# Optimization experiments

Measured on AMD Instinct MI355X. Metric: run time of the kernel, lower is better.

The kernel has to match this reference:

```python
import jax, jax.numpy as jnp
import numpy as np

# Hyperparameters from init_kwargs
K = 1024           # num_embeddings
D = 256            # embedding_dim
COMMIT = 0.25      # commitment_cost
DECAY = 0.99
LAMBDA = 1e-05
NU = 0.1
TAU = 0.5


def setup_inputs() -> dict:
    key = jax.random.key(0)
    k1, k2, k3 = jax.random.split(key, 3)
    B, H, W = 32, 32, 32
    N = B * H * W
    inputs = jax.random.normal(k1, (B, D, H, W), jnp.float32)
    weight = jax.random.normal(k2, (K, D), jnp.float32) * 0.02  # codebook
    # EMA buffers as initialized on first training step (non-kmeans branch)
    ema_count = jnp.full((K,), N / K, jnp.float32)
    ema_weight = weight * ema_count[:, None]
    # Gumbel noise used by F.gumbel_softmax(-distances, tau, hard=True)
    gumbel_noise = jax.random.gumbel(k3, (N, K), jnp.float32)
    return {"inputs": inputs, "weight": weight, "ema_count": ema_count,
            "ema_weight": ema_weight, "gumbel_noise": gumbel_noise}


def reference(inputs, weight, ema_count, ema_weight, gumbel_noise):
    B, C, H, W = inputs.shape
    # b d h w -> (b h w) d
    x = jnp.transpose(inputs, (0, 2, 3, 1)).reshape(-1, C)  # [N, D]
    N = x.shape[0]

    distances = (jnp.sum(x * x, axis=1, keepdims=True)
                 + jnp.sum(weight * weight, axis=1)
                 - 2.0 * jnp.einsum('nd,kd->nk', x, weight))

    soft_encodings = jax.nn.softmax(-distances / TAU, axis=-1)  # [N, K]

    # Hard gumbel-softmax sample (computed under no_grad in torch):
    # argmax((logits + g)/tau) == argmax(logits + g), logits = -distances
    idx = jnp.argmax(-distances + gumbel_noise, axis=-1)        # [N]
    encodings = jax.nn.one_hot(idx, K, dtype=x.dtype)           # [N, K]

    quantized = (encodings @ weight).reshape(B, H, W, C)        # [B,H,W,D]

    # EMA codebook update (training branch, no_grad)
    new_count = ema_count * DECAY + jnp.sum(soft_encodings, axis=0) * (1.0 - DECAY)
    new_count = (new_count + LAMBDA) / (N + K * LAMBDA) * N
    d_weight = jnp.einsum('nk,nd->kd', soft_encodings, x)
    new_ema_weight = ema_weight * DECAY + d_weight * (1.0 - DECAY)
    new_embedding = new_ema_weight / new_count[:, None]

    # Negative-entropy commitment loss on soft assignments
    probs = soft_encodings
    loss_latents = jnp.mean(jnp.sum(probs * jnp.log(jnp.clip(probs, 1e-08)), axis=-1))
    loss = COMMIT * loss_latents

    # quantized + nu*(quantized - detach(quantized)) == quantized in value
    quantized = quantized + NU * (quantized - jax.lax.stop_gradient(quantized))

    avg_probs = jnp.mean(encodings, axis=0)
    perplexity = jnp.exp(-jnp.sum(avg_probs * jnp.log(avg_probs + 1e-10)))

    quantized_out = jnp.transpose(quantized, (0, 3, 1, 2))  # [B,D,H,W]
    return (loss, quantized_out, perplexity, encodings,
            new_count, new_ema_weight, new_embedding)
```

## Files before the change

kernel.cpp:

```cpp
#include <hip/hip_runtime.h>
#include <math.h>

#define NROWS 32768
#define KCB   1024
#define DDIM  256
#define NHALF 16384

#define O_LOSS 0
#define O_Q    1
#define O_PERP 8388609
#define O_ENC  8388610
#define O_NCNT 41943042
#define O_EMAW 41944066
#define O_EMB  42206210

#define E_XS3   2
#define E_S     12582914

#define W_WSQ  0
#define W_XSQ  1024
#define W_IDX  33792
#define W_COL  66560
#define W_HCNT 67584
#define W_BENT 68608
#define W_NCNT 76800
#define W_T2I  77824
#define W_WB   143360

typedef __attribute__((ext_vector_type(8))) short bf16x8;
typedef __attribute__((ext_vector_type(4))) float f32x4;

#define GLOAD_LDS16(g, l) __builtin_amdgcn_global_load_lds( \
    (const __attribute__((address_space(1))) unsigned int*)(g), \
    (__attribute__((address_space(3))) unsigned int*)(l), 16, 0, 0)

__device__ __forceinline__ float wred_sum(float v) {
#pragma unroll
  for (int off = 32; off > 0; off >>= 1) v += __shfl_xor(v, off);
  return v;
}
__device__ __forceinline__ ushort f2bf(float f) {
  union { float f; unsigned u; } c; c.f = f;
  unsigned u = c.u;
  return (ushort)((u + 0x7fffu + ((u >> 16) & 1u)) >> 16);
}
__device__ __forceinline__ float bf2f(ushort h) {
  union { unsigned u; float f; } c; c.u = ((unsigned)h) << 16;
  return c.f;
}

__global__ void k_init(float* __restrict__ hcnt) {
  int i = blockIdx.x * 256 + threadIdx.x;
  if (i < 1024) hcnt[i] = 0.f;
}

__global__ void k_wsplit(const float* __restrict__ w, float* __restrict__ wsq,
                         ushort* __restrict__ WB) {
  int t = threadIdx.x;
  int lane = t & 63, wv = t >> 6;
  int k = blockIdx.x * 4 + wv;
  int d0 = lane * 4;
  float4 v = *(const float4*)&w[(size_t)k * DDIM + d0];
  float s = v.x * v.x + v.y * v.y + v.z * v.z + v.w * v.w;
  s = wred_sum(s);
  if (lane == 0) wsq[k] = s;
  float vv[4] = {v.x, v.y, v.z, v.w};
  union { ushort u[4]; uint2 q; } hh, mm;
#pragma unroll
  for (int q = 0; q < 4; ++q) {
    ushort h = f2bf(vv[q]);
    float r = vv[q] - bf2f(h);
    hh.u[q] = h;
    mm.u[q] = f2bf(r);
  }
  ushort* row = WB + (size_t)k * 768;
  *(uint2*)&row[d0] = hh.q;
  *(uint2*)&row[256 + d0] = hh.q;
  *(uint2*)&row[512 + d0] = mm.q;
}

__global__ __launch_bounds__(256) void k_xsplit(const float* __restrict__ x,
                                                ushort* __restrict__ XS3,
                                                float* __restrict__ xsq) {
  __shared__ __align__(16) ushort sl[32 * 776];
  __shared__ float sq[32 * 9];
  int t = threadIdx.x;
  int b = blockIdx.x >> 5, mt = blockIdx.x & 31;
  int m0 = mt * 32, mloc = t & 31, dgrp = t >> 5;
  const float* xb = x + (size_t)b * DDIM * 1024 + m0 + mloc;
  float s = 0.f;
#pragma unroll
  for (int jj = 0; jj < 8; ++jj) {
    int d0 = dgrp * 32 + jj * 4;
    float vv[4];
#pragma unroll
    for (int q = 0; q < 4; ++q) vv[q] = xb[(size_t)(d0 + q) * 1024];
    union { ushort u[4]; uint2 q; } hh, mi, lo;
#pragma unroll
    for (int q = 0; q < 4; ++q) {
      float v = vv[q];
      ushort h = f2bf(v);
      float r1 = v - bf2f(h);
      ushort m_ = f2bf(r1);
      float r2 = r1 - bf2f(m_);
      hh.u[q] = h; mi.u[q] = m_; lo.u[q] = f2bf(r2);
      s = fmaf(v, v, s);
    }
    int base = mloc * 776;
    *(uint2*)&sl[base + d0] = hh.q;
    *(uint2*)&sl[base + 256 + d0] = mi.q;
    *(uint2*)&sl[base + 512 + d0] = lo.q;
  }
  sq[mloc * 9 + dgrp] = s;
  __syncthreads();
  if (t < 32) {
    float ss = 0.f;
#pragma unroll
    for (int gq = 0; gq < 8; ++gq) ss += sq[t * 9 + gq];
    xsq[b * 1024 + m0 + t] = ss;
  }
  ushort* dst = XS3 + (size_t)(b * 1024 + m0) * 768;
#pragma unroll
  for (int p = 0; p < 12; ++p) {
    int idx = p * 256 + t;
    int row = idx / 96;
    int co = idx - row * 96;
    *(uint4*)&dst[(size_t)row * 768 + co * 8] = *(uint4*)&sl[row * 776 + co * 8];
  }
}

__global__ __launch_bounds__(256) void k_gemm1t(const ushort* __restrict__ XS3h,
                                                const ushort* __restrict__ WB,
                                                const float* __restrict__ wsq,
                                                const float* __restrict__ xsqh,
                                                float* __restrict__ S) {
  __shared__ __align__(16) ushort Asl[2][8192];
  __shared__ __align__(16) ushort Bsl[2][8192];
  __shared__ float xsl[128];
  __shared__ float wsl[128];
  int t = threadIdx.x;
  int kt = blockIdx.x;
  int n0 = blockIdx.y * 128;
  int k0 = kt * 128;
  int l = t & 63, wid = t >> 6;
  int wr = wid >> 1, wc = wid & 1;
  int hi = l >> 4, c = l & 15;

  if (t < 128) { xsl[t] = xsqh[n0 + t]; wsl[t] = wsq[k0 + t]; }

  f32x4 zero = {0.f, 0.f, 0.f, 0.f};
  f32x4 acc[4][4];
#pragma unroll
  for (int i = 0; i < 4; ++i)
#pragma unroll
    for (int j = 0; j < 4; ++j) acc[i][j] = zero;

  const char* XSb = (const char*)XS3h;
  const char* WBb = (const char*)WB;
  int lr = l >> 3;
  int lsw = ((l & 7) ^ lr) << 4;

#define STAGE(s_, b_)                                                              \
  {                                                                                \
    size_t bofs_ = (size_t)(s_) << 7;                                              \
    size_t aofs_ = (size_t)(((s_) < 8) ? (s_) : (s_) - 8) << 7;                    \
    char* Ad_ = (char*)Asl + (b_) * 16384;                                         \
    char* Bd_ = (char*)Bsl + (b_) * 16384;                                         \
    _Pragma("unroll")                                                              \
    for (int q_ = 0; q_ < 4; ++q_) {                                               \
      int seg_ = wid * 32 + q_ * 8;                                                \
      GLOAD_LDS16(XSb + (size_t)(n0 + seg_ + lr) * 1536 + aofs_ + lsw,             \
                  Ad_ + seg_ * 128);                                               \
      GLOAD_LDS16(WBb + (size_t)(k0 + seg_ + lr) * 1536 + bofs_ + lsw,             \
                  Bd_ + seg_ * 128);                                               \
    }                                                                              \
  }

  STAGE(0, 0);
  asm volatile("s_waitcnt vmcnt(0)" ::: "memory");
  __builtin_amdgcn_s_barrier();
  __builtin_amdgcn_sched_barrier(0);

  int buf = 0;
  for (int s = 0; s < 12; ++s) {
    if (s < 11) STAGE(s + 1, buf ^ 1);
    const ushort* Ab = &Asl[buf][0];
    const ushort* Bb = &Bsl[buf][0];
#pragma unroll
    for (int kk = 0; kk < 2; ++kk) {
      bf16x8 af[4], bg[4];
#pragma unroll
      for (int i = 0; i < 4; ++i) {
        int row = wr * 64 + i * 16 + c;
        int ch = (kk * 4 + hi) ^ (row & 7);
        af[i] = *(const bf16x8*)&Ab[row * 64 + ch * 8];
      }
#pragma unroll
      for (int j = 0; j < 4; ++j) {
        int row = wc * 64 + j * 16 + c;
        int ch = (kk * 4 + hi) ^ (row & 7);
        bg[j] = *(const bf16x8*)&Bb[row * 64 + ch * 8];
      }
#pragma unroll
      for (int i = 0; i < 4; ++i)
#pragma unroll
        for (int j = 0; j < 4; ++j)
          acc[i][j] = __builtin_amdgcn_mfma_f32_16x16x32_bf16(af[i], bg[j], acc[i][j], 0, 0, 0);
    }
    asm volatile("s_waitcnt vmcnt(0)" ::: "memory");
    __builtin_amdgcn_s_barrier();
    buf ^= 1;
  }
#undef STAGE

#pragma unroll
  for (int i = 0; i < 4; ++i) {
#pragma unroll
    for (int r = 0; r < 4; ++r) {
      int nl = wr * 64 + i * 16 + hi * 4 + r;
      float xs = xsl[nl];
#pragma unroll
      for (int j = 0; j < 4; ++j) {
        int kl = wc * 64 + j * 16 + c;
        float nd = fmaf(2.f, acc[i][j][r], -(xs + wsl[kl]));
        S[(size_t)(n0 + nl) * 1024 + k0 + kl] = nd;
      }
    }
  }
}

__global__ __launch_bounds__(256) void k_rowops2(float* __restrict__ S,
                                                 const float* __restrict__ Gh,
                                                 float* __restrict__ benth,
                                                 int* __restrict__ t2igh) {
  __shared__ float went[4];
  int t = threadIdx.x;
  int l = t & 63, wv = t >> 6;
  int n = blockIdx.x * 4 + wv;
  float* row = S + ((size_t)n << 10);
  const float* grow = Gh + ((size_t)n << 10);
  float v[16];
  float mx = -3.0e38f;
  float v1 = -3.0e38f, v2 = -3.0e38f;
  int i1 = 0x7fffffff, i2 = 0x7fffffff;
#pragma unroll
  for (int j = 0; j < 4; ++j) {
    float4 a = *(const float4*)&row[j * 256 + l * 4];
    float4 gg = *(const float4*)&grow[j * 256 + l * 4];
    float av[4] = {a.x, a.y, a.z, a.w};
    float gv[4] = {gg.x, gg.y, gg.z, gg.w};
#pragma unroll
    for (int q = 0; q < 4; ++q) {
      v[j * 4 + q] = av[q];
      mx = fmaxf(mx, av[q]);
      float sc = av[q] + gv[q];
      int kk = j * 256 + l * 4 + q;
      if (sc > v1 || (sc == v1 && kk < i1)) { v2 = v1; i2 = i1; v1 = sc; i1 = kk; }
      else if (sc > v2 || (sc == v2 && kk < i2)) { v2 = sc; i2 = kk; }
    }
  }
#pragma unroll
  for (int off = 1; off < 64; off <<= 1) {
    mx = fmaxf(mx, __shfl_xor(mx, off));
    float ov1 = __shfl_xor(v1, off), ov2 = __shfl_xor(v2, off);
    int oi1 = __shfl_xor(i1, off), oi2 = __shfl_xor(i2, off);
    bool fB = (ov1 > v1) || (ov1 == v1 && oi1 < i1);
    float nv1 = fB ? ov1 : v1; int ni1 = fB ? oi1 : i1;
    float ca = fB ? v1 : ov1;  int cia = fB ? i1 : oi1;
    float cb = fB ? ov2 : v2;  int cib = fB ? oi2 : i2;
    bool sB = (cb > ca) || (cb == ca && cib < cia);
    v1 = nv1; i1 = ni1;
    v2 = sB ? cb : ca; i2 = sB ? cib : cia;
  }
  if (l == 0) { t2igh[n * 2] = i1; t2igh[n * 2 + 1] = i2; }

  float M = 2.f * mx;
  float e[16]; float ps = 0.f;
#pragma unroll
  for (int u = 0; u < 16; ++u) { e[u] = __expf(fmaf(2.f, v[u], -M)); ps += e[u]; }
  ps = wred_sum(ps);
  float inv = 1.f / ps;
  float ent = 0.f;
#pragma unroll
  for (int j = 0; j < 4; ++j) {
    float4 o;
    float s0 = e[j * 4 + 0] * inv, s1 = e[j * 4 + 1] * inv;
    float s2 = e[j * 4 + 2] * inv, s3 = e[j * 4 + 3] * inv;
    ent += s0 * __logf(fmaxf(s0, 1e-8f)) + s1 * __logf(fmaxf(s1, 1e-8f));
    ent += s2 * __logf(fmaxf(s2, 1e-8f)) + s3 * __logf(fmaxf(s3, 1e-8f));
    o.x = s0; o.y = s1; o.z = s2; o.w = s3;
    *(float4*)&row[j * 256 + l * 4] = o;
  }
  ent = wred_sum(ent);
  if (l == 0) went[wv] = ent;
  __syncthreads();
  if (t == 0) benth[blockIdx.x] = went[0] + went[1] + went[2] + went[3];
}

__global__ void k_transpose2(const float* __restrict__ soft, ushort* __restrict__ sTp) {
  __shared__ ushort lds[64 * 65];
  int t = threadIdx.x;
  int ktile = blockIdx.x & 15, nt = blockIdx.x >> 4;
  int n0 = nt * 64, k0 = ktile * 64;
#pragma unroll
  for (int p = 0; p < 2; ++p) {
    int row = p * 32 + (t >> 3);
    int c8 = (t & 7) * 8;
    float4 a = *(const float4*)&soft[(size_t)(n0 + row) * 1024 + k0 + c8];
    float4 b = *(const float4*)&soft[(size_t)(n0 + row) * 1024 + k0 + c8 + 4];
    ushort* d = &lds[row * 65 + c8];
    d[0] = f2bf(a.x); d[1] = f2bf(a.y); d[2] = f2bf(a.z); d[3] = f2bf(a.w);
    d[4] = f2bf(b.x); d[5] = f2bf(b.y); d[6] = f2bf(b.z); d[7] = f2bf(b.w);
  }
  __syncthreads();
#pragma unroll
  for (int p = 0; p < 2; ++p) {
    int krow = p * 32 + (t >> 3);
    int nc8 = (t & 7) * 8;
    uint* dst = (uint*)&sTp[(size_t)(k0 + krow) * NHALF + n0 + nc8];
#pragma unroll
    for (int j = 0; j < 4; ++j) {
      uint lo = lds[(nc8 + 2 * j) * 65 + krow];
      uint hh = lds[(nc8 + 2 * j + 1) * 65 + krow];
      dst[j] = lo | (hh << 16);
    }
  }
}

__global__ __launch_bounds__(256) void k_refine(const ushort* __restrict__ XS3,
                                                const float* __restrict__ w,
                                                const float* __restrict__ wsq,
                                                const float* __restrict__ xsq,
                                                const float* __restrict__ G,
                                                const int* __restrict__ t2ig,
                                                int* __restrict__ idxArr,
                                                float* __restrict__ hcnt) {
  int t = threadIdx.x;
  int l = t & 63, wv = t >> 6;
  int base = blockIdx.x * 64 + wv * 16;
  int d0 = l * 4;
  for (int rr = 0; rr < 16; ++rr) {
    int n = base + rr;
    const ushort* p = XS3 + (size_t)n * 768;
    union { uint2 q; ushort u[4]; } ha, ma, la;
    ha.q = *(const uint2*)&p[d0];
    ma.q = *(const uint2*)&p[256 + d0];
    la.q = *(const uint2*)&p[512 + d0];
    float xv[4];
#pragma unroll
    for (int q = 0; q < 4; ++q) xv[q] = bf2f(ha.u[q]) + bf2f(ma.u[q]) + bf2f(la.u[q]);
    float xs = xsq[n];
    int ia = t2ig[n * 2], ib = t2ig[n * 2 + 1];
    float sc[2];
    int ids[2] = {ia, ib};
#pragma unroll
    for (int cdd = 0; cdd < 2; ++cdd) {
      int id = ids[cdd];
      const float* wr = w + (size_t)id * DDIM;
      float4 wv4 = *(const float4*)&wr[d0];
      float d = xv[0] * wv4.x + xv[1] * wv4.y + xv[2] * wv4.z + xv[3] * wv4.w;
      d = wred_sum(d);
      sc[cdd] = fmaf(2.f, d, -xs) - wsq[id] + G[((size_t)n << 10) + id];
    }
    int win = (sc[1] > sc[0] || (sc[1] == sc[0] && ib < ia)) ? ib : ia;
    if (l == 0) {
      idxArr[n] = win;
      atomicAdd(&hcnt[win], 1.f);
    }
  }
}

__global__ void k_quant(const float* __restrict__ w, const int* __restrict__ idxArr,
                        float* __restrict__ outQ) {
  int n = blockIdx.x * 256 + threadIdx.x;
  int b = n >> 10, m = n & 1023;
  int id = idxArr[n];
  const float* wr = w + (size_t)id * DDIM;
  float* o = outQ + (size_t)b * DDIM * 1024 + m;
#pragma unroll 4
  for (int d = 0; d < DDIM; ++d) o[(size_t)d * 1024] = wr[d];
}

__global__ __launch_bounds__(512) void k_gemm2_mfma(const ushort* __restrict__ sT0,
                                                    const ushort* __restrict__ sT1,
                                                    const float* __restrict__ x,
                                                    float* __restrict__ P) {
  __shared__ __align__(16) ushort Abuf[256 * 72];
  __shared__ __align__(16) ushort Bbuf[128 * 72];
  int t = threadIdx.x;
  int bid = blockIdx.x;
  int kt = bid & 3, dt = (bid >> 2) & 1, ns = bid >> 3;
  int k0 = kt * 256, d0 = dt * 128;
  int l = t & 63, wv = t >> 6;
  int wk = wv >> 1, wd = wv & 1;
  const ushort* Abase = (ns < 16) ? sT0 : sT1;
  size_t nloc0 = (size_t)(ns & 15) * 1024;
  f32x4 zero = {0.f, 0.f, 0.f, 0.f};
  f32x4 acc[4][4];
#pragma unroll
  for (int i = 0; i < 4; ++i)
#pragma unroll
    for (int j = 0; j < 4; ++j) acc[i][j] = zero;

  int colv = (t & 7) * 8;
  int rbase = t >> 3;
  for (int s = 0; s < 16; ++s) {
#pragma unroll
    for (int p = 0; p < 4; ++p) {
      int row = p * 64 + rbase;
      const uint* ap = (const uint*)(Abase + (size_t)(k0 + row) * NHALF + nloc0 + s * 64 + colv);
      uint4 v; v.x = ap[0]; v.y = ap[1]; v.z = ap[2]; v.w = ap[3];
      *(uint4*)&Abuf[row * 72 + colv] = v;
    }
#pragma unroll
    for (int p = 0; p < 2; ++p) {
      int row = p * 64 + rbase;
      const float* xp = &x[((size_t)ns * DDIM + d0 + row) * 1024 + s * 64 + colv];
      float4 a = *(const float4*)xp;
      float4 b = *(const float4*)(xp + 4);
      union { ushort u[8]; uint4 q; } pk;
      pk.u[0] = f2bf(a.x); pk.u[1] = f2bf(a.y); pk.u[2] = f2bf(a.z); pk.u[3] = f2bf(a.w);
      pk.u[4] = f2bf(b.x); pk.u[5] = f2bf(b.y); pk.u[6] = f2bf(b.z); pk.u[7] = f2bf(b.w);
      *(uint4*)&Bbuf[row * 72 + colv] = pk.q;
    }
    __syncthreads();
    bf16x8 af[4], bfr[4];
#pragma unroll
    for (int nb2 = 0; nb2 < 2; ++nb2) {
#pragma unroll
      for (int sub = 0; sub < 4; ++sub) {
        af[sub] = *(const bf16x8*)&Abuf[(wk * 64 + sub * 16 + (l & 15)) * 72 + nb2 * 32 + (l >> 4) * 8];
        bfr[sub] = *(const bf16x8*)&Bbuf[(wd * 64 + sub * 16 + (l & 15)) * 72 + nb2 * 32 + (l >> 4) * 8];
      }
#pragma unroll
      for (int i = 0; i < 4; ++i)
#pragma unroll
        for (int j = 0; j < 4; ++j)
          acc[i][j] = __builtin_amdgcn_mfma_f32_16x16x32_bf16(af[i], bfr[j], acc[i][j], 0, 0, 0);
    }
    __syncthreads();
  }
  float* Pb = P + (size_t)ns * (KCB * DDIM);
#pragma unroll
  for (int i = 0; i < 4; ++i)
#pragma unroll
    for (int j = 0; j < 4; ++j) {
#pragma unroll
      for (int r = 0; r < 4; ++r) {
        int k = k0 + wk * 64 + i * 16 + (l >> 4) * 4 + r;
        int d = d0 + wd * 64 + j * 16 + (l & 15);
        Pb[(size_t)k * DDIM + d] = acc[i][j][r];
      }
    }
}

__global__ void k_colsum2(const ushort* __restrict__ sT0, const ushort* __restrict__ sT1,
                          float* __restrict__ colsum) {
  int k = blockIdx.x;
  int t = threadIdx.x;
  const uint* r0 = (const uint*)(sT0 + (size_t)k * NHALF);
  const uint* r1 = (const uint*)(sT1 + (size_t)k * NHALF);
  float s = 0.f;
#pragma unroll
  for (int cc = 0; cc < 8; ++cc) {
#pragma unroll
    for (int q = 0; q < 4; ++q) {
      uint a = r0[cc * 1024 + t * 4 + q];
      uint b = r1[cc * 1024 + t * 4 + q];
      s += bf2f((ushort)(a & 0xffffu)) + bf2f((ushort)(a >> 16));
      s += bf2f((ushort)(b & 0xffffu)) + bf2f((ushort)(b >> 16));
    }
  }
  s = wred_sum(s);
  __shared__ float ws4[4];
  if ((t & 63) == 0) ws4[t >> 6] = s;
  __syncthreads();
  if (t == 0) colsum[k] = ws4[0] + ws4[1] + ws4[2] + ws4[3];
}

__global__ void k_final1(const float* __restrict__ ema_count, const float* __restrict__ colsum,
                         const float* __restrict__ hcnt, const float* __restrict__ bent,
                         float* __restrict__ ncnt, float* __restrict__ out) {
  __shared__ float red[1024];
  int t = threadIdx.x;
  const float onem = 1.0f - 0.99f;
  float nc = ema_count[t] * 0.99f + colsum[t] * onem;
  nc = (nc + 1e-5f) / (32768.0f + 1024.0f * 1e-5f) * 32768.0f;
  out[O_NCNT + t] = nc;
  ncnt[t] = nc;
  float s = 0.f;
  for (int i = t; i < 8192; i += 1024) s += bent[i];
  red[t] = s;
  __syncthreads();
  for (int off = 512; off > 0; off >>= 1) { if (t < off) red[t] += red[t + off]; __syncthreads(); }
  if (t == 0) out[O_LOSS] = 0.25f * (red[0] / 32768.0f);
  __syncthreads();
  float avg = hcnt[t] * (1.0f / 32768.0f);
  red[t] = avg * logf(avg + 1e-10f);
  __syncthreads();
  for (int off = 512; off > 0; off >>= 1) { if (t < off) red[t] += red[t + off]; __syncthreads(); }
  if (t == 0) out[O_PERP] = expf(-red[0]);
}

__global__ void k_reduce_final2(const float* __restrict__ P, const float* __restrict__ ema_w,
                                const float* __restrict__ ncnt, float* __restrict__ outEW,
                                float* __restrict__ outEMB) {
  int i = blockIdx.x * 256 + threadIdx.x;
  float s = 0.f;
#pragma unroll
  for (int ns = 0; ns < 32; ++ns) s += P[(size_t)ns * (KCB * DDIM) + i];
  float ew = ema_w[i] * 0.99f + s * 0.01f;
  outEW[i] = ew;
  outEMB[i] = ew / ncnt[i >> 8];
}

__global__ void k_onehot(const int* __restrict__ idxArr, float* __restrict__ E) {
  int gid = blockIdx.x * 256 + threadIdx.x;
  int n = gid >> 8;
  int k4 = (gid & 255) * 4;
  int id = idxArr[n];
  float2* E2 = (float2*)E;
  size_t base = ((size_t)n * KCB + k4) >> 1;
  float2 vA = {(float)(k4 == id), (float)(k4 + 1 == id)};
  float2 vB = {(float)(k4 + 2 == id), (float)(k4 + 3 == id)};
  E2[base] = vA;
  E2[base + 1] = vB;
}

extern "C" void kernel_launch(void* const* d_in, const int* in_sizes, int n_in,
                              void* d_out, int out_size, void* d_ws, size_t ws_size,
                              hipStream_t stream) {
  const float* x = (const float*)d_in[0];
  const float* w = (const float*)d_in[1];
  const float* ema_count = (const float*)d_in[2];
  const float* ema_w = (const float*)d_in[3];
  const float* g = (const float*)d_in[4];
  float* out = (float*)d_out;
  float* ws = (float*)d_ws;

  float* wsq    = ws + W_WSQ;
  float* xsq    = ws + W_XSQ;
  int*   idxArr = (int*)(ws + W_IDX);
  float* colsum = ws + W_COL;
  float* hcnt   = ws + W_HCNT;
  float* bent   = ws + W_BENT;
  float* ncnt   = ws + W_NCNT;
  int*   top2i  = (int*)(ws + W_T2I);
  ushort* WB    = (ushort*)(ws + W_WB);

  float* outQ = out + O_Q;
  float* outE = out + O_ENC;

  ushort* XS3    = (ushort*)(outE + E_XS3);
  float*  Sslot  = outE + E_S;
  ushort* softT1 = (ushort*)(outE + E_XS3);
  ushort* softT0 = (ushort*)outQ;

  k_init<<<4, 256, 0, stream>>>(hcnt);
  k_wsplit<<<256, 256, 0, stream>>>(w, wsq, WB);
  k_xsplit<<<1024, 256, 0, stream>>>(x, XS3, xsq);
  k_gemm1t<<<dim3(8, 128), 256, 0, stream>>>(XS3, WB, wsq, xsq, Sslot);
  k_rowops2<<<4096, 256, 0, stream>>>(Sslot, g, bent, top2i);
  k_transpose2<<<4096, 256, 0, stream>>>(Sslot, softT0);
  k_gemm1t<<<dim3(8, 128), 256, 0, stream>>>(XS3 + (size_t)NHALF * 768, WB,
                                             wsq, xsq + NHALF, Sslot);
  k_rowops2<<<4096, 256, 0, stream>>>(Sslot, g + (size_t)NHALF * 1024,
                                      bent + 4096, top2i + NHALF * 2);
  k_refine<<<512, 256, 0, stream>>>(XS3, w, wsq, xsq, g, top2i, idxArr, hcnt);
  k_transpose2<<<4096, 256, 0, stream>>>(Sslot, softT1);
  k_colsum2<<<1024, 256, 0, stream>>>(softT0, softT1, colsum);
  k_gemm2_mfma<<<256, 512, 0, stream>>>(softT0, softT1, x, Sslot);
  k_final1<<<1, 1024, 0, stream>>>(ema_count, colsum, hcnt, bent, ncnt, out);
  k_reduce_final2<<<1024, 256, 0, stream>>>(Sslot, ema_w, ncnt, out + O_EMAW, out + O_EMB);
  k_quant<<<128, 256, 0, stream>>>(w, idxArr, outQ);
  k_onehot<<<32768, 256, 0, stream>>>(idxArr, outE);
}
```

Before: 402.6 us.

## Drop weight-residual split in distance GEMM and recompute softmax during transpose

```diff
diff --git a/kernel.cpp b/kernel.cpp
--- a/kernel.cpp
+++ b/kernel.cpp
@@ -26,6 +26,8 @@
 #define W_NCNT 76800
 #define W_T2I  77824
 #define W_WB   143360
+#define W_MROW 274432
+#define W_IROW 307200
 
 typedef __attribute__((ext_vector_type(8))) short bf16x8;
 typedef __attribute__((ext_vector_type(4))) float f32x4;
@@ -65,18 +67,10 @@
   s = wred_sum(s);
   if (lane == 0) wsq[k] = s;
   float vv[4] = {v.x, v.y, v.z, v.w};
-  union { ushort u[4]; uint2 q; } hh, mm;
-#pragma unroll
-  for (int q = 0; q < 4; ++q) {
-    ushort h = f2bf(vv[q]);
-    float r = vv[q] - bf2f(h);
-    hh.u[q] = h;
-    mm.u[q] = f2bf(r);
-  }
-  ushort* row = WB + (size_t)k * 768;
-  *(uint2*)&row[d0] = hh.q;
-  *(uint2*)&row[256 + d0] = hh.q;
-  *(uint2*)&row[512 + d0] = mm.q;
+  union { ushort u[4]; uint2 q; } hh;
+#pragma unroll
+  for (int q = 0; q < 4; ++q) hh.u[q] = f2bf(vv[q]);
+  *(uint2*)&WB[(size_t)k * 256 + d0] = hh.q;
 }
 
 __global__ __launch_bounds__(256) void k_xsplit(const float* __restrict__ x,
@@ -162,8 +156,9 @@
 
 #define STAGE(s_, b_)                                                              \
   {                                                                                \
-    size_t bofs_ = (size_t)(s_) << 7;                                              \
-    size_t aofs_ = (size_t)(((s_) < 8) ? (s_) : (s_) - 8) << 7;                    \
+    size_t bofs_ = (size_t)((s_) & 3) << 7;                                        \
+    size_t aofs_ = ((s_) < 4) ? ((size_t)(s_) << 7)                                \
+                              : (size_t)(512 + (((s_) - 4) << 7));                 \
     char* Ad_ = (char*)Asl + (b_) * 16384;                                         \
     char* Bd_ = (char*)Bsl + (b_) * 16384;                                         \
     _Pragma("unroll")                                                              \
@@ -171,7 +166,7 @@
       int seg_ = wid * 32 + q_ * 8;                                                \
       GLOAD_LDS16(XSb + (size_t)(n0 + seg_ + lr) * 1536 + aofs_ + lsw,             \
                   Ad_ + seg_ * 128);                                               \
-      GLOAD_LDS16(WBb + (size_t)(k0 + seg_ + lr) * 1536 + bofs_ + lsw,             \
+      GLOAD_LDS16(WBb + (size_t)(k0 + seg_ + lr) * 512 + bofs_ + lsw,              \
                   Bd_ + seg_ * 128);                                               \
     }                                                                              \
   }
@@ -182,8 +177,8 @@
   __builtin_amdgcn_sched_barrier(0);
 
   int buf = 0;
-  for (int s = 0; s < 12; ++s) {
-    if (s < 11) STAGE(s + 1, buf ^ 1);
+  for (int s = 0; s < 8; ++s) {
+    if (s < 7) STAGE(s + 1, buf ^ 1);
     const ushort* Ab = &Asl[buf][0];
     const ushort* Bb = &Bsl[buf][0];
 #pragma unroll
@@ -229,15 +224,17 @@
   }
 }
 
-__global__ __launch_bounds__(256) void k_rowops2(float* __restrict__ S,
+__global__ __launch_bounds__(256) void k_rowstat(const float* __restrict__ S,
                                                  const float* __restrict__ Gh,
+                                                 float* __restrict__ Mrowh,
+                                                 float* __restrict__ Irowh,
                                                  float* __restrict__ benth,
                                                  int* __restrict__ t2igh) {
   __shared__ float went[4];
   int t = threadIdx.x;
   int l = t & 63, wv = t >> 6;
   int n = blockIdx.x * 4 + wv;
-  float* row = S + ((size_t)n << 10);
+  const float* row = S + ((size_t)n << 10);
   const float* grow = Gh + ((size_t)n << 10);
   float v[16];
   float mx = -3.0e38f;
@@ -272,8 +269,6 @@
     v1 = nv1; i1 = ni1;
     v2 = sB ? cb : ca; i2 = sB ? cib : cia;
   }
-  if (l == 0) { t2igh[n * 2] = i1; t2igh[n * 2 + 1] = i2; }
-
   float M = 2.f * mx;
   float e[16]; float ps = 0.f;
 #pragma unroll
@@ -282,41 +277,44 @@
   float inv = 1.f / ps;
   float ent = 0.f;
 #pragma unroll
-  for (int j = 0; j < 4; ++j) {
-    float4 o;
-    float s0 = e[j * 4 + 0] * inv, s1 = e[j * 4 + 1] * inv;
-    float s2 = e[j * 4 + 2] * inv, s3 = e[j * 4 + 3] * inv;
-    ent += s0 * __logf(fmaxf(s0, 1e-8f)) + s1 * __logf(fmaxf(s1, 1e-8f));
-    ent += s2 * __logf(fmaxf(s2, 1e-8f)) + s3 * __logf(fmaxf(s3, 1e-8f));
-    o.x = s0; o.y = s1; o.z = s2; o.w = s3;
-    *(float4*)&row[j * 256 + l * 4] = o;
+  for (int u = 0; u < 16; ++u) {
+    float sfv = e[u] * inv;
+    ent += sfv * __logf(fmaxf(sfv, 1e-8f));
   }
   ent = wred_sum(ent);
-  if (l == 0) went[wv] = ent;
+  if (l == 0) {
+    t2igh[n * 2] = i1; t2igh[n * 2 + 1] = i2;
+    Mrowh[n] = M; Irowh[n] = inv;
+    went[wv] = ent;
+  }
   __syncthreads();
   if (t == 0) benth[blockIdx.x] = went[0] + went[1] + went[2] + went[3];
 }
 
-__global__ void k_transpose2(const float* __restrict__ soft, ushort* __restrict__ sTp) {
+__global__ __launch_bounds__(512) void k_rowwrite(const float* __restrict__ S,
+                                                  const float* __restrict__ Mrowh,
+                                                  const float* __restrict__ Irowh,
+                                                  ushort* __restrict__ sTp) {
   __shared__ ushort lds[64 * 65];
-  int t = threadIdx.x;
-  int ktile = blockIdx.x & 15, nt = blockIdx.x >> 4;
-  int n0 = nt * 64, k0 = ktile * 64;
-#pragma unroll
-  for (int p = 0; p < 2; ++p) {
-    int row = p * 32 + (t >> 3);
-    int c8 = (t & 7) * 8;
-    float4 a = *(const float4*)&soft[(size_t)(n0 + row) * 1024 + k0 + c8];
-    float4 b = *(const float4*)&soft[(size_t)(n0 + row) * 1024 + k0 + c8 + 4];
+  __shared__ float Ml[64], Il[64];
+  int t = threadIdx.x;
+  int n0 = blockIdx.x * 64;
+  if (t < 64) { Ml[t] = Mrowh[n0 + t]; Il[t] = Irowh[n0 + t]; }
+  __syncthreads();
+  for (int kt = 0; kt < 16; ++kt) {
+    int k0 = kt * 64;
+    int row = t >> 3, c8 = (t & 7) * 8;
+    float M = Ml[row], inv = Il[row];
+    const float* sp = &S[(size_t)(n0 + row) * 1024 + k0 + c8];
+    float4 a = *(const float4*)sp;
+    float4 b = *(const float4*)(sp + 4);
+    float sv[8] = {a.x, a.y, a.z, a.w, b.x, b.y, b.z, b.w};
     ushort* d = &lds[row * 65 + c8];
-    d[0] = f2bf(a.x); d[1] = f2bf(a.y); d[2] = f2bf(a.z); d[3] = f2bf(a.w);
-    d[4] = f2bf(b.x); d[5] = f2bf(b.y); d[6] = f2bf(b.z); d[7] = f2bf(b.w);
-  }
-  __syncthreads();
-#pragma unroll
-  for (int p = 0; p < 2; ++p) {
-    int krow = p * 32 + (t >> 3);
-    int nc8 = (t & 7) * 8;
+#pragma unroll
+    for (int j = 0; j < 8; ++j)
+      d[j] = f2bf(__expf(fmaf(2.f, sv[j], -M)) * inv);
+    __syncthreads();
+    int krow = t >> 3, nc8 = (t & 7) * 8;
     uint* dst = (uint*)&sTp[(size_t)(k0 + krow) * NHALF + n0 + nc8];
 #pragma unroll
     for (int j = 0; j < 4; ++j) {
@@ -324,6 +322,7 @@
       uint hh = lds[(nc8 + 2 * j + 1) * 65 + krow];
       dst[j] = lo | (hh << 16);
     }
+    __syncthreads();
   }
 }
 
@@ -547,6 +546,8 @@
   float* ncnt   = ws + W_NCNT;
   int*   top2i  = (int*)(ws + W_T2I);
   ushort* WB    = (ushort*)(ws + W_WB);
+  float* Mrow   = ws + W_MROW;
+  float* Irow   = ws + W_IROW;
 
   float* outQ = out + O_Q;
   float* outE = out + O_ENC;
@@ -560,14 +561,15 @@
   k_wsplit<<<256, 256, 0, stream>>>(w, wsq, WB);
   k_xsplit<<<1024, 256, 0, stream>>>(x, XS3, xsq);
   k_gemm1t<<<dim3(8, 128), 256, 0, stream>>>(XS3, WB, wsq, xsq, Sslot);
-  k_rowops2<<<4096, 256, 0, stream>>>(Sslot, g, bent, top2i);
-  k_transpose2<<<4096, 256, 0, stream>>>(Sslot, softT0);
+  k_rowstat<<<4096, 256, 0, stream>>>(Sslot, g, Mrow, Irow, bent, top2i);
+  k_rowwrite<<<256, 512, 0, stream>>>(Sslot, Mrow, Irow, softT0);
   k_gemm1t<<<dim3(8, 128), 256, 0, stream>>>(XS3 + (size_t)NHALF * 768, WB,
                                              wsq, xsq + NHALF, Sslot);
-  k_rowops2<<<4096, 256, 0, stream>>>(Sslot, g + (size_t)NHALF * 1024,
+  k_rowstat<<<4096, 256, 0, stream>>>(Sslot, g + (size_t)NHALF * 1024,
+                                      Mrow + NHALF, Irow + NHALF,
                                       bent + 4096, top2i + NHALF * 2);
   k_refine<<<512, 256, 0, stream>>>(XS3, w, wsq, xsq, g, top2i, idxArr, hcnt);
-  k_transpose2<<<4096, 256, 0, stream>>>(Sslot, softT1);
+  k_rowwrite<<<256, 512, 0, stream>>>(Sslot, Mrow + NHALF, Irow + NHALF, softT1);
   k_colsum2<<<1024, 256, 0, stream>>>(softT0, softT1, colsum);
   k_gemm2_mfma<<<256, 512, 0, stream>>>(softT0, softT1, x, Sslot);
   k_final1<<<1, 1024, 0, stream>>>(ema_count, colsum, hcnt, bent, ncnt, out);
```

Result: faster. 359.6 us (-10.7%).
